# Kernel optimization log

Hardware: AMD Instinct MI355X
Metric: run time of the kernel (lower is better)

The kernel has to match this reference:

```python
import jax, jax.numpy as jnp
import numpy as np

V, B, P = 32, 128, 256   # views/directions, batch, max points per diagram
J = 75                   # n_elements (structure elements)
NF = 32                  # n_filters (= directions)
S2 = 25                  # stage_2_out
NU = 0.1
BN_EPS = 1e-5


def _transform(births, lifetimes):
    """UpperDiagonalThresholdedLogTransform(nu=0.1) on (birth, death) points."""
    deaths = births + lifetimes + 0.01
    inv = jnp.asarray(1.0 / np.sqrt(2.0), births.dtype)
    x = (births + deaths) * inv          # rotated 1st coord
    y = (deaths - births) * inv          # rotated 2nd coord (persistence), > 0
    y = jnp.where(y <= NU, jnp.log(y / NU) * NU + NU, y)
    return jnp.stack([x, y], axis=-1)    # [V,B,P,2]


def _batchnorm(x, gamma, beta, axis):
    mean = x.mean(axis=axis, keepdims=True)
    var = x.var(axis=axis, keepdims=True)  # biased, training-mode BN
    return (x - mean) / jnp.sqrt(var + BN_EPS) * gamma + beta


def setup_inputs() -> dict:
    key = jax.random.key(0)
    ks = jax.random.split(key, 20)
    inp = {
        "births": jax.random.uniform(ks[0], (V, B, P), jnp.float32),
        "lifetimes": jax.random.uniform(ks[1], (V, B, P), jnp.float32),
        "mask": jax.random.randint(ks[2], (V, B, P), 0, 2).astype(jnp.int32),
        # SLayerPHT params (one SLayer per view)
        "centers": jax.random.uniform(ks[3], (V, J, 2), jnp.float32),
        "sharpness": 4.0 + 0.1 * jax.random.normal(ks[4], (V, J, 2), jnp.float32),
        # stage_1: Conv1d(3->NF, k=1, no bias), Conv1d(NF->8, k=1, no bias)
        "w1": 0.1 * jax.random.normal(ks[5], (V, NF, 3), jnp.float32),
        "w2": 0.1 * jax.random.normal(ks[6], (V, 8, NF), jnp.float32),
        # stage_2: Linear(J->S2), BN(S2), Linear(S2->S2)
        "l1_w": 0.1 * jax.random.normal(ks[7], (V, S2, J), jnp.float32),
        "l1_b": 0.1 * jax.random.normal(ks[8], (V, S2), jnp.float32),
        "bn1_g": jnp.ones((V, S2), jnp.float32),
        "bn1_b": jnp.zeros((V, S2), jnp.float32),
        "l2_w": 0.1 * jax.random.normal(ks[9], (V, S2, S2), jnp.float32),
        "l2_b": 0.1 * jax.random.normal(ks[10], (V, S2), jnp.float32),
        # linear_1: Linear(V*S2 -> 500) + BN(500); linear_2: Linear(500 -> 200)
        "fc1_w": 0.05 * jax.random.normal(ks[11], (500, V * S2), jnp.float32),
        "fc1_b": 0.05 * jax.random.normal(ks[12], (500,), jnp.float32),
        "bn2_g": jnp.ones((500,), jnp.float32),
        "bn2_b": jnp.zeros((500,), jnp.float32),
        "fc2_w": 0.05 * jax.random.normal(ks[13], (200, 500), jnp.float32),
        "fc2_b": 0.05 * jax.random.normal(ks[14], (200,), jnp.float32),
    }
    return inp


def reference(births, lifetimes, mask, centers, sharpness, w1, w2,
              l1_w, l1_b, bn1_g, bn1_b, l2_w, l2_b,
              fc1_w, fc1_b, bn2_g, bn2_b, fc2_w, fc2_b):
    q = _transform(births, lifetimes)                 # [V,B,P,2]
    m = mask.astype(q.dtype)                          # [V,B,P]
    # SLayer: z[v,b,j] = sum_p m * exp(-sum_d s[v,j,d]^2 (q[v,b,p,d]-c[v,j,d])^2)
    s2 = sharpness * sharpness                        # [V,J,2]
    qa = jnp.concatenate([q * q, q, jnp.ones_like(q[..., :1])], axis=-1)  # [V,B,P,5]
    ca = jnp.concatenate([s2, -2.0 * s2 * centers,
                          (s2 * centers * centers).sum(-1, keepdims=True)], axis=-1)  # [V,J,5]
    d2 = jnp.einsum('vbpk,vjk->vbpj', qa, ca)         # squared weighted distance
    z = jnp.einsum('vbpj,vbp->vbj', jnp.exp(-d2), m)  # [V,B,J]
    # neighbor-direction stacking (n_neighbor_directions=1, cyclic): [i-1, i, i+1]
    zn = jnp.stack([jnp.roll(z, 1, axis=0), z, jnp.roll(z, -1, axis=0)], axis=2)  # [V,B,3,J]
    # stage_1: two 1x1 conv1d (no bias), then max over channels
    h = jnp.einsum('vbcj,vfc->vbfj', zn, w1)          # [V,B,NF,J]
    h = jnp.einsum('vbfj,vgf->vbgj', h, w2)           # [V,B,8,J]
    h = h.max(axis=2)                                 # [V,B,J]
    # stage_2: Linear -> BN(train) -> Linear -> ReLU (Dropout = eval identity)
    u = jnp.einsum('vbj,voj->vbo', h, l1_w) + l1_b[:, None, :]   # [V,B,S2]
    u = _batchnorm(u, bn1_g[:, None, :], bn1_b[:, None, :], axis=1)
    u = jnp.einsum('vbo,vpo->vbp', u, l2_w) + l2_b[:, None, :]
    u = jax.nn.relu(u)
    x = u.transpose(1, 0, 2).reshape(B, V * S2)       # torch.cat(x, 1)
    x = x @ fc1_w.T + fc1_b
    x = _batchnorm(x, bn2_g, bn2_b, axis=0)
    x = x @ fc2_w.T + fc2_b                           # [B,200]
    return x
```

## Files before the change

### kernel.cpp

```cpp
#include <hip/hip_runtime.h>

#define V 32
#define B 128
#define P 256
#define J 75
#define NF 32
#define S2 25

__global__ __launch_bounds__(128) void slayer_kernel(
    const float* __restrict__ births,
    const float* __restrict__ lifetimes,
    const int* __restrict__ mask,
    const float* __restrict__ centers,
    const float* __restrict__ sharpness,
    float* __restrict__ z)
{
    const int vb = blockIdx.x;
    const int v  = vb >> 7;
    const int tid = threadIdx.x;
    const int lane = tid & 63;

    __shared__ float4 pts[P];
    __shared__ int cnt;

    if (tid == 0) cnt = 0;
    __syncthreads();

    const float inv = 0.70710678118654752f;
    #pragma unroll
    for (int c = 0; c < 2; ++c) {
        const int p  = tid + c * 128;
        const int gi = vb * P + p;
        float b0 = births[gi];
        float l0 = lifetimes[gi];
        int   m  = mask[gi];
        float d  = b0 + l0 + 0.01f;
        float x  = (b0 + d) * inv;
        float y  = (d - b0) * inv;
        if (y <= 0.1f) y = __logf(y * 10.0f) * 0.1f + 0.1f;

        bool keep = (m != 0);
        unsigned long long bal = __ballot(keep);
        unsigned long long lt  = (1ull << lane) - 1ull;
        int prefix = __popcll(bal & lt);
        int total  = __popcll(bal);
        int base = 0;
        if (lane == 0) base = atomicAdd(&cnt, total);
        base = __shfl(base, 0, 64);
        if (keep) pts[base + prefix] = make_float4(x, y, x * x, y * y);
    }
    __syncthreads();

    const int n = cnt;
    if (tid < J) {
        const int cj = (v * J + tid) * 2;
        float cx = centers[cj + 0];
        float cy = centers[cj + 1];
        float sx = sharpness[cj + 0];
        float sy = sharpness[cj + 1];
        float s2x = sx * sx, s2y = sy * sy;
        float k0 = -s2x;
        float k1 = -s2y;
        float k2 = 2.0f * s2x * cx;
        float k3 = 2.0f * s2y * cy;
        float kc = -(s2x * cx * cx + s2y * cy * cy);
        float acc = 0.f;
        #pragma unroll 4
        for (int p = 0; p < n; ++p) {
            float4 a = pts[p];
            float d = fmaf(k0, a.z, kc);
            d = fmaf(k1, a.w, d);
            d = fmaf(k2, a.x, d);
            d = fmaf(k3, a.y, d);
            acc += __expf(d);
        }
        z[vb * J + tid] = acc;
    }
}

__global__ __launch_bounds__(128) void stage12_kernel(
    const float* __restrict__ z,
    const float* __restrict__ w1,
    const float* __restrict__ w2,
    const float* __restrict__ l1_w,
    const float* __restrict__ l1_b,
    float* __restrict__ u_pre)
{
    const int vb = blockIdx.x;
    const int v  = vb >> 7;
    const int b  = vb & 127;
    const int vm = (v + V - 1) & (V - 1);
    const int vp = (v + 1) & (V - 1);
    const int tid = threadIdx.x;

    __shared__ float z0[J], z1[J], z2[J];
    __shared__ float w1s[NF * 3];
    __shared__ float w2s[8 * NF];
    __shared__ float hsh[J];

    if (tid < J) {
        z0[tid] = z[(vm * B + b) * J + tid];
        z1[tid] = z[(v  * B + b) * J + tid];
        z2[tid] = z[(vp * B + b) * J + tid];
    }
    if (tid < NF * 3) w1s[tid] = w1[v * NF * 3 + tid];
    w2s[tid]       = w2[v * 8 * NF + tid];
    w2s[tid + 128] = w2[v * 8 * NF + tid + 128];
    __syncthreads();

    if (tid < J) {
        float a0 = z0[tid], a1 = z1[tid], a2 = z2[tid];
        float hf[NF];
        #pragma unroll
        for (int f = 0; f < NF; ++f)
            hf[f] = w1s[f * 3 + 0] * a0 + w1s[f * 3 + 1] * a1 + w1s[f * 3 + 2] * a2;
        float hm = -3.4e38f;
        #pragma unroll
        for (int g = 0; g < 8; ++g) {
            float s = 0.f;
            #pragma unroll
            for (int f = 0; f < NF; ++f) s += w2s[g * NF + f] * hf[f];
            hm = fmaxf(hm, s);
        }
        hsh[tid] = hm;
    }
    __syncthreads();

    if (tid < S2) {
        float acc = l1_b[v * S2 + tid];
        const float* wrow = l1_w + (v * S2 + tid) * J;
        for (int j = 0; j < J; ++j) acc += hsh[j] * wrow[j];
        u_pre[vb * S2 + tid] = acc;
    }
}

__global__ __launch_bounds__(256) void bn1_l2_kernel(
    const float* __restrict__ u_pre,
    const float* __restrict__ bn1_g,
    const float* __restrict__ bn1_b,
    const float* __restrict__ l2_w,
    const float* __restrict__ l2_b,
    float* __restrict__ xT)
{
    const int v = blockIdx.x;
    const int tid = threadIdx.x;

    __shared__ float u[B * S2];
    __shared__ float w[S2 * S2];
    __shared__ float sc[S2], sh[S2];

    for (int i = tid; i < B * S2; i += 256) u[i] = u_pre[v * B * S2 + i];
    for (int i = tid; i < S2 * S2; i += 256) w[i] = l2_w[v * S2 * S2 + i];
    __syncthreads();

    if (tid < S2) {
        float s = 0.f, ss = 0.f;
        for (int b = 0; b < B; ++b) {
            float x = u[b * S2 + tid];
            s += x; ss += x * x;
        }
        float mean = s * (1.f / B);
        float var  = ss * (1.f / B) - mean * mean;
        float istd = rsqrtf(var + 1e-5f);
        float g  = bn1_g[v * S2 + tid];
        float be = bn1_b[v * S2 + tid];
        sc[tid] = g * istd;
        sh[tid] = be - mean * g * istd;
    }
    __syncthreads();

    for (int i = tid; i < B * S2; i += 256) {
        int o = i % S2;
        u[i] = u[i] * sc[o] + sh[o];
    }
    __syncthreads();

    for (int i = tid; i < B * S2; i += 256) {
        int b = i & 127;
        int p = i >> 7;
        float acc = l2_b[v * S2 + p];
        #pragma unroll
        for (int o = 0; o < S2; ++o) acc += u[b * S2 + o] * w[p * S2 + o];
        acc = fmaxf(acc, 0.f);
        xT[(v * S2 + p) * B + b] = acc;
    }
}

#define FC1_TILE 2
__global__ __launch_bounds__(128) void fc1_bn2_kernel(
    const float* __restrict__ xT,
    const float* __restrict__ fc1_w,
    const float* __restrict__ fc1_b,
    const float* __restrict__ bn2_g,
    const float* __restrict__ bn2_b,
    float* __restrict__ y1n)
{
    const int n0 = blockIdx.x * FC1_TILE;
    const int tid = threadIdx.x;
    const int K = V * S2;

    __shared__ float wsm[FC1_TILE][V * S2];
    __shared__ float red[2][2][FC1_TILE];

    for (int i = tid; i < FC1_TILE * K; i += 128) {
        int ni = i / K;
        int k  = i - ni * K;
        wsm[ni][k] = fc1_w[(n0 + ni) * K + k];
    }
    __syncthreads();

    float acc[FC1_TILE] = {0.f, 0.f};
    for (int k = 0; k < K; ++k) {
        float xv = xT[k * B + tid];
        #pragma unroll
        for (int ni = 0; ni < FC1_TILE; ++ni) acc[ni] += xv * wsm[ni][k];
    }

    const int wave = tid >> 6;
    const int lane = tid & 63;
    #pragma unroll
    for (int ni = 0; ni < FC1_TILE; ++ni) {
        acc[ni] += fc1_b[n0 + ni];
        float s = acc[ni], ss = acc[ni] * acc[ni];
        #pragma unroll
        for (int off = 32; off > 0; off >>= 1) {
            s  += __shfl_down(s,  off, 64);
            ss += __shfl_down(ss, off, 64);
        }
        if (lane == 0) { red[wave][0][ni] = s; red[wave][1][ni] = ss; }
    }
    __syncthreads();

    #pragma unroll
    for (int ni = 0; ni < FC1_TILE; ++ni) {
        float s  = red[0][0][ni] + red[1][0][ni];
        float ss = red[0][1][ni] + red[1][1][ni];
        float mean = s * (1.f / B);
        float var  = ss * (1.f / B) - mean * mean;
        float istd = rsqrtf(var + 1e-5f);
        float g  = bn2_g[n0 + ni];
        float be = bn2_b[n0 + ni];
        float scl = g * istd;
        y1n[(n0 + ni) * B + tid] = acc[ni] * scl + (be - mean * scl);
    }
}

__global__ __launch_bounds__(128) void fc2_kernel(
    const float* __restrict__ y1n,
    const float* __restrict__ fc2_w,
    const float* __restrict__ fc2_b,
    float* __restrict__ out)
{
    const int k = blockIdx.x;
    const int tid = threadIdx.x;

    __shared__ float wsm[500];
    for (int i = tid; i < 500; i += 128) wsm[i] = fc2_w[k * 500 + i];
    __syncthreads();

    float acc = fc2_b[k];
    for (int n = 0; n < 500; ++n) acc += y1n[n * B + tid] * wsm[n];
    out[tid * 200 + k] = acc;
}

extern "C" void kernel_launch(void* const* d_in, const int* in_sizes, int n_in,
                              void* d_out, int out_size, void* d_ws, size_t ws_size,
                              hipStream_t stream) {
    const float* births    = (const float*)d_in[0];
    const float* lifetimes = (const float*)d_in[1];
    const int*   mask      = (const int*)d_in[2];
    const float* centers   = (const float*)d_in[3];
    const float* sharpness = (const float*)d_in[4];
    const float* w1        = (const float*)d_in[5];
    const float* w2        = (const float*)d_in[6];
    const float* l1_w      = (const float*)d_in[7];
    const float* l1_b      = (const float*)d_in[8];
    const float* bn1_g     = (const float*)d_in[9];
    const float* bn1_b     = (const float*)d_in[10];
    const float* l2_w      = (const float*)d_in[11];
    const float* l2_b      = (const float*)d_in[12];
    const float* fc1_w     = (const float*)d_in[13];
    const float* fc1_b     = (const float*)d_in[14];
    const float* bn2_g     = (const float*)d_in[15];
    const float* bn2_b     = (const float*)d_in[16];
    const float* fc2_w     = (const float*)d_in[17];
    const float* fc2_b     = (const float*)d_in[18];
    float* out = (float*)d_out;

    float* ws    = (float*)d_ws;
    float* z     = ws;
    float* u_pre = ws + 307200;
    float* xT    = ws + 307200 + 102400;
    float* y1n   = ws + 307200 + 102400 + 102400;

    slayer_kernel <<<V * B, 128, 0, stream>>>(births, lifetimes, mask, centers, sharpness, z);
    stage12_kernel<<<V * B, 128, 0, stream>>>(z, w1, w2, l1_w, l1_b, u_pre);
    bn1_l2_kernel <<<V, 256, 0, stream>>>(u_pre, bn1_g, bn1_b, l2_w, l2_b, xT);
    fc1_bn2_kernel<<<(500 / FC1_TILE), 128, 0, stream>>>(xT, fc1_w, fc1_b, bn2_g, bn2_b, y1n);
    fc2_kernel    <<<200, 128, 0, stream>>>(y1n, fc2_w, fc2_b, out);
}
```

Measured before the change: 184.0 us.

## Fuse post-SLayer stages into one cooperative kernel with grid syncs

Replaces the four kernels after the SLayer stage with a single cooperative kernel of 256 blocks that runs stage1/2, BN1+linear2, fc1+BN2 and fc2, separated by grid.sync barriers. Each block now handles 16 batch rows of one view and keeps the view's l1 weights in shared memory, instead of one block per (view, batch) re-reading them. fc1 and fc2 each compute two outputs per 256-thread block. The aim is to remove three launch gaps and the repeated weight loads, at the cost of grid-wide barriers and low occupancy in phases where only a few blocks (for example 32 in the BN1 phase) do work.

```diff
diff --git a/kernel.cpp b/kernel.cpp
--- a/kernel.cpp
+++ b/kernel.cpp
@@ -1,4 +1,7 @@
 #include <hip/hip_runtime.h>
+#include <hip/hip_cooperative_groups.h>
+
+namespace cg = cooperative_groups;
 
 #define V 32
 #define B 128
@@ -78,189 +81,196 @@
     }
 }
 
-__global__ __launch_bounds__(128) void stage12_kernel(
+__global__ __launch_bounds__(256, 1) void fused_rest_kernel(
     const float* __restrict__ z,
     const float* __restrict__ w1,
     const float* __restrict__ w2,
     const float* __restrict__ l1_w,
     const float* __restrict__ l1_b,
-    float* __restrict__ u_pre)
-{
-    const int vb = blockIdx.x;
-    const int v  = vb >> 7;
-    const int b  = vb & 127;
-    const int vm = (v + V - 1) & (V - 1);
-    const int vp = (v + 1) & (V - 1);
-    const int tid = threadIdx.x;
-
-    __shared__ float z0[J], z1[J], z2[J];
-    __shared__ float w1s[NF * 3];
-    __shared__ float w2s[8 * NF];
-    __shared__ float hsh[J];
-
-    if (tid < J) {
-        z0[tid] = z[(vm * B + b) * J + tid];
-        z1[tid] = z[(v  * B + b) * J + tid];
-        z2[tid] = z[(vp * B + b) * J + tid];
-    }
-    if (tid < NF * 3) w1s[tid] = w1[v * NF * 3 + tid];
-    w2s[tid]       = w2[v * 8 * NF + tid];
-    w2s[tid + 128] = w2[v * 8 * NF + tid + 128];
-    __syncthreads();
-
-    if (tid < J) {
-        float a0 = z0[tid], a1 = z1[tid], a2 = z2[tid];
-        float hf[NF];
-        #pragma unroll
-        for (int f = 0; f < NF; ++f)
-            hf[f] = w1s[f * 3 + 0] * a0 + w1s[f * 3 + 1] * a1 + w1s[f * 3 + 2] * a2;
-        float hm = -3.4e38f;
-        #pragma unroll
-        for (int g = 0; g < 8; ++g) {
-            float s = 0.f;
-            #pragma unroll
-            for (int f = 0; f < NF; ++f) s += w2s[g * NF + f] * hf[f];
-            hm = fmaxf(hm, s);
-        }
-        hsh[tid] = hm;
-    }
-    __syncthreads();
-
-    if (tid < S2) {
-        float acc = l1_b[v * S2 + tid];
-        const float* wrow = l1_w + (v * S2 + tid) * J;
-        for (int j = 0; j < J; ++j) acc += hsh[j] * wrow[j];
-        u_pre[vb * S2 + tid] = acc;
-    }
-}
-
-__global__ __launch_bounds__(256) void bn1_l2_kernel(
-    const float* __restrict__ u_pre,
     const float* __restrict__ bn1_g,
     const float* __restrict__ bn1_b,
     const float* __restrict__ l2_w,
     const float* __restrict__ l2_b,
-    float* __restrict__ xT)
-{
-    const int v = blockIdx.x;
-    const int tid = threadIdx.x;
-
-    __shared__ float u[B * S2];
-    __shared__ float w[S2 * S2];
-    __shared__ float sc[S2], sh[S2];
-
-    for (int i = tid; i < B * S2; i += 256) u[i] = u_pre[v * B * S2 + i];
-    for (int i = tid; i < S2 * S2; i += 256) w[i] = l2_w[v * S2 * S2 + i];
-    __syncthreads();
-
-    if (tid < S2) {
-        float s = 0.f, ss = 0.f;
-        for (int b = 0; b < B; ++b) {
-            float x = u[b * S2 + tid];
-            s += x; ss += x * x;
-        }
-        float mean = s * (1.f / B);
-        float var  = ss * (1.f / B) - mean * mean;
-        float istd = rsqrtf(var + 1e-5f);
-        float g  = bn1_g[v * S2 + tid];
-        float be = bn1_b[v * S2 + tid];
-        sc[tid] = g * istd;
-        sh[tid] = be - mean * g * istd;
-    }
-    __syncthreads();
-
-    for (int i = tid; i < B * S2; i += 256) {
-        int o = i % S2;
-        u[i] = u[i] * sc[o] + sh[o];
-    }
-    __syncthreads();
-
-    for (int i = tid; i < B * S2; i += 256) {
-        int b = i & 127;
-        int p = i >> 7;
-        float acc = l2_b[v * S2 + p];
-        #pragma unroll
-        for (int o = 0; o < S2; ++o) acc += u[b * S2 + o] * w[p * S2 + o];
-        acc = fmaxf(acc, 0.f);
-        xT[(v * S2 + p) * B + b] = acc;
-    }
-}
-
-#define FC1_TILE 2
-__global__ __launch_bounds__(128) void fc1_bn2_kernel(
-    const float* __restrict__ xT,
     const float* __restrict__ fc1_w,
     const float* __restrict__ fc1_b,
     const float* __restrict__ bn2_g,
     const float* __restrict__ bn2_b,
-    float* __restrict__ y1n)
+    const float* __restrict__ fc2_w,
+    const float* __restrict__ fc2_b,
+    float* __restrict__ u_pre,
+    float* __restrict__ xT,
+    float* __restrict__ y1n,
+    float* __restrict__ out)
 {
-    const int n0 = blockIdx.x * FC1_TILE;
+    const int bb  = blockIdx.x;
     const int tid = threadIdx.x;
-    const int K = V * S2;
-
-    __shared__ float wsm[FC1_TILE][V * S2];
-    __shared__ float red[2][2][FC1_TILE];
-
-    for (int i = tid; i < FC1_TILE * K; i += 128) {
-        int ni = i / K;
-        int k  = i - ni * K;
-        wsm[ni][k] = fc1_w[(n0 + ni) * K + k];
-    }
-    __syncthreads();
-
-    float acc[FC1_TILE] = {0.f, 0.f};
-    for (int k = 0; k < K; ++k) {
-        float xv = xT[k * B + tid];
-        #pragma unroll
-        for (int ni = 0; ni < FC1_TILE; ++ni) acc[ni] += xv * wsm[ni][k];
-    }
-
-    const int wave = tid >> 6;
-    const int lane = tid & 63;
-    #pragma unroll
-    for (int ni = 0; ni < FC1_TILE; ++ni) {
-        acc[ni] += fc1_b[n0 + ni];
-        float s = acc[ni], ss = acc[ni] * acc[ni];
+    cg::grid_group grid = cg::this_grid();
+
+    __shared__ float w1s[NF * 3];
+    __shared__ float w2s[8 * NF];
+    __shared__ float l1ws[S2 * J];
+    __shared__ float l1bs[S2];
+    __shared__ float zsh[3][3 * J];
+    __shared__ float hshA[3 * J];
+    __shared__ float ub[B * S2];
+    __shared__ float wb[S2 * S2];
+    __shared__ float scb[S2], shb[S2];
+    __shared__ float wc[2][V * S2];
+    __shared__ float redc[4][2];
+    __shared__ float wd[2 * 500];
+
+    {
+        const int v  = bb >> 3;
+        const int b0 = (bb & 7) * 16;
+        const int vm = (v + V - 1) & (V - 1);
+        const int vp = (v + 1) & (V - 1);
+
+        if (tid < NF * 3) w1s[tid] = w1[v * NF * 3 + tid];
+        if (tid < 8 * NF) w2s[tid] = w2[v * 8 * NF + tid];
+        for (int i = tid; i < S2 * J; i += 256) l1ws[i] = l1_w[v * S2 * J + i];
+        if (tid < S2) l1bs[tid] = l1_b[v * S2 + tid];
+        __syncthreads();
+
+        for (int bi = 0; bi < 16; bi += 3) {
+            const int nb = min(3, 16 - bi);
+            for (int i = tid; i < nb * 3 * J; i += 256) {
+                int bl    = i / (3 * J);
+                int r     = i - bl * (3 * J);
+                int which = r / J;
+                int j     = r - which * J;
+                int b     = b0 + bi + bl;
+                int vsrc  = (which == 0) ? vm : ((which == 1) ? v : vp);
+                zsh[bl][which * J + j] = z[(vsrc * B + b) * J + j];
+            }
+            __syncthreads();
+
+            if (tid < nb * J) {
+                int bl = tid / J;
+                int j  = tid - bl * J;
+                float a0 = zsh[bl][0 * J + j];
+                float a1 = zsh[bl][1 * J + j];
+                float a2 = zsh[bl][2 * J + j];
+                float hf[NF];
+                #pragma unroll
+                for (int f = 0; f < NF; ++f)
+                    hf[f] = w1s[f * 3 + 0] * a0 + w1s[f * 3 + 1] * a1 + w1s[f * 3 + 2] * a2;
+                float hm = -3.4e38f;
+                #pragma unroll
+                for (int g = 0; g < 8; ++g) {
+                    float s = 0.f;
+                    #pragma unroll
+                    for (int f = 0; f < NF; ++f) s += w2s[g * NF + f] * hf[f];
+                    hm = fmaxf(hm, s);
+                }
+                hshA[bl * J + j] = hm;
+            }
+            __syncthreads();
+
+            if (tid < nb * S2) {
+                int bl = tid / S2;
+                int o  = tid - bl * S2;
+                float acc = l1bs[o];
+                for (int j = 0; j < J; ++j) acc += hshA[bl * J + j] * l1ws[o * J + j];
+                u_pre[(v * B + b0 + bi + bl) * S2 + o] = acc;
+            }
+            __syncthreads();
+        }
+    }
+
+    grid.sync();
+
+    if (bb < V) {
+        const int v = bb;
+        for (int i = tid; i < B * S2; i += 256) ub[i] = u_pre[v * B * S2 + i];
+        for (int i = tid; i < S2 * S2; i += 256) wb[i] = l2_w[v * S2 * S2 + i];
+        __syncthreads();
+
+        if (tid < S2) {
+            float s = 0.f, ss = 0.f;
+            for (int b = 0; b < B; ++b) {
+                float x = ub[b * S2 + tid];
+                s += x; ss += x * x;
+            }
+            float mean = s * (1.f / B);
+            float var  = ss * (1.f / B) - mean * mean;
+            float istd = rsqrtf(var + 1e-5f);
+            float g  = bn1_g[v * S2 + tid];
+            float be = bn1_b[v * S2 + tid];
+            scb[tid] = g * istd;
+            shb[tid] = be - mean * g * istd;
+        }
+        __syncthreads();
+
+        for (int i = tid; i < B * S2; i += 256) {
+            int o = i % S2;
+            ub[i] = ub[i] * scb[o] + shb[o];
+        }
+        __syncthreads();
+
+        for (int i = tid; i < B * S2; i += 256) {
+            int b = i & 127;
+            int p = i >> 7;
+            float acc = l2_b[v * S2 + p];
+            #pragma unroll
+            for (int o = 0; o < S2; ++o) acc += ub[b * S2 + o] * wb[p * S2 + o];
+            acc = fmaxf(acc, 0.f);
+            xT[(v * S2 + p) * B + b] = acc;
+        }
+    }
+
+    grid.sync();
+
+    if (bb < 250) {
+        const int n0 = bb * 2;
+        const int K  = V * S2;
+        for (int i = tid; i < 2 * K; i += 256) {
+            int ni = i / K;
+            int k  = i - ni * K;
+            wc[ni][k] = fc1_w[(n0 + ni) * K + k];
+        }
+        __syncthreads();
+
+        const int ni = tid >> 7;
+        const int b  = tid & 127;
+        float acc = 0.f;
+        for (int k = 0; k < K; ++k) acc += xT[k * B + b] * wc[ni][k];
+        acc += fc1_b[n0 + ni];
+
+        const int wave = tid >> 6;
+        const int lane = tid & 63;
+        float s = acc, ss = acc * acc;
         #pragma unroll
         for (int off = 32; off > 0; off >>= 1) {
             s  += __shfl_down(s,  off, 64);
             ss += __shfl_down(ss, off, 64);
         }
-        if (lane == 0) { red[wave][0][ni] = s; red[wave][1][ni] = ss; }
-    }
-    __syncthreads();
-
-    #pragma unroll
-    for (int ni = 0; ni < FC1_TILE; ++ni) {
-        float s  = red[0][0][ni] + red[1][0][ni];
-        float ss = red[0][1][ni] + red[1][1][ni];
-        float mean = s * (1.f / B);
-        float var  = ss * (1.f / B) - mean * mean;
+        if (lane == 0) { redc[wave][0] = s; redc[wave][1] = ss; }
+        __syncthreads();
+
+        float sT  = redc[2 * ni][0] + redc[2 * ni + 1][0];
+        float ssT = redc[2 * ni][1] + redc[2 * ni + 1][1];
+        float mean = sT * (1.f / B);
+        float var  = ssT * (1.f / B) - mean * mean;
         float istd = rsqrtf(var + 1e-5f);
-        float g  = bn2_g[n0 + ni];
-        float be = bn2_b[n0 + ni];
+        float g   = bn2_g[n0 + ni];
+        float be  = bn2_b[n0 + ni];
         float scl = g * istd;
-        y1n[(n0 + ni) * B + tid] = acc[ni] * scl + (be - mean * scl);
-    }
-}
-
-__global__ __launch_bounds__(128) void fc2_kernel(
-    const float* __restrict__ y1n,
-    const float* __restrict__ fc2_w,
-    const float* __restrict__ fc2_b,
-    float* __restrict__ out)
-{
-    const int k = blockIdx.x;
-    const int tid = threadIdx.x;
-
-    __shared__ float wsm[500];
-    for (int i = tid; i < 500; i += 128) wsm[i] = fc2_w[k * 500 + i];
-    __syncthreads();
-
-    float acc = fc2_b[k];
-    for (int n = 0; n < 500; ++n) acc += y1n[n * B + tid] * wsm[n];
-    out[tid * 200 + k] = acc;
+        y1n[(n0 + ni) * B + b] = acc * scl + (be - mean * scl);
+    }
+
+    grid.sync();
+
+    if (bb < 100) {
+        for (int i = tid; i < 2 * 500; i += 256) wd[i] = fc2_w[bb * 2 * 500 + i];
+        __syncthreads();
+
+        const int ni = tid >> 7;
+        const int b  = tid & 127;
+        const int k  = bb * 2 + ni;
+        float acc = fc2_b[k];
+        for (int n = 0; n < 500; ++n) acc += y1n[n * B + b] * wd[ni * 500 + n];
+        out[b * 200 + k] = acc;
+    }
 }
 
 extern "C" void kernel_launch(void* const* d_in, const int* in_sizes, int n_in,
@@ -293,9 +303,15 @@
     float* xT    = ws + 307200 + 102400;
     float* y1n   = ws + 307200 + 102400 + 102400;
 
-    slayer_kernel <<<V * B, 128, 0, stream>>>(births, lifetimes, mask, centers, sharpness, z);
-    stage12_kernel<<<V * B, 128, 0, stream>>>(z, w1, w2, l1_w, l1_b, u_pre);
-    bn1_l2_kernel <<<V, 256, 0, stream>>>(u_pre, bn1_g, bn1_b, l2_w, l2_b, xT);
-    fc1_bn2_kernel<<<(500 / FC1_TILE), 128, 0, stream>>>(xT, fc1_w, fc1_b, bn2_g, bn2_b, y1n);
-    fc2_kernel    <<<200, 128, 0, stream>>>(y1n, fc2_w, fc2_b, out);
+    slayer_kernel<<<V * B, 128, 0, stream>>>(births, lifetimes, mask, centers, sharpness, z);
+
+    void* args[] = {
+        (void*)&z, (void*)&w1, (void*)&w2, (void*)&l1_w, (void*)&l1_b,
+        (void*)&bn1_g, (void*)&bn1_b, (void*)&l2_w, (void*)&l2_b,
+        (void*)&fc1_w, (void*)&fc1_b, (void*)&bn2_g, (void*)&bn2_b,
+        (void*)&fc2_w, (void*)&fc2_b,
+        (void*)&u_pre, (void*)&xT, (void*)&y1n, (void*)&out
+    };
+    hipLaunchCooperativeKernel((const void*)fused_rest_kernel,
+                               dim3(256), dim3(256), args, 0, stream);
 }
```

Result: slower. 599.9 us (+226.0%).
